# Performance work log

Measured on AMD Instinct MI355X. Metric: run time of the kernel, lower is better.

Reference implementation:

```python
import jax, jax.numpy as jnp
import numpy as np

N_NODES = 50000
N_EDGES = 800000
D_IN = 128
D_HID = 128


def _sage_conv(x, src, dst, W_l, b_l, W_r, num_nodes):
    # PyG SAGEConv (mean aggr): out = lin_l(mean_{j in N(i)} x_j) + lin_r(x_i)
    msgs = x[src]  # [E, d] irregular gather
    agg = jax.ops.segment_sum(msgs, dst, num_segments=num_nodes)  # [N, d]
    cnt = jax.ops.segment_sum(jnp.ones((dst.shape[0], 1), x.dtype), dst, num_segments=num_nodes)
    agg = agg / jnp.maximum(cnt, 1.0)  # mean over in-neighbors
    return agg @ W_l.T + b_l + x @ W_r.T


def setup_inputs() -> dict:
    key = jax.random.key(0)
    ks = jax.random.split(key, 8)
    x = jax.random.normal(ks[0], (N_NODES, D_IN), dtype=jnp.float32)
    edge_index = jax.random.randint(ks[1], (2, N_EDGES), 0, N_NODES, dtype=jnp.int64)
    s0 = 1.0 / np.sqrt(D_IN)
    s1 = 1.0 / np.sqrt(D_HID)
    return {
        "x": x,
        "edge_index": edge_index,
        "W_l0": jax.random.uniform(ks[2], (D_HID, D_IN), jnp.float32, -s0, s0),
        "b_l0": jnp.zeros((D_HID,), jnp.float32),
        "W_r0": jax.random.uniform(ks[3], (D_HID, D_IN), jnp.float32, -s0, s0),
        "W_l1": jax.random.uniform(ks[4], (D_HID, D_HID), jnp.float32, -s1, s1),
        "b_l1": jnp.zeros((D_HID,), jnp.float32),
        "W_r1": jax.random.uniform(ks[5], (D_HID, D_HID), jnp.float32, -s1, s1),
    }


def reference(x, edge_index, W_l0, b_l0, W_r0, W_l1, b_l1, W_r1):
    src, dst = edge_index[0], edge_index[1]
    n = x.shape[0]
    # layer 0 + ReLU (dropout is identity at inference)
    h = _sage_conv(x, src, dst, W_l0, b_l0, W_r0, n)
    h = jax.nn.relu(h)
    # layer 1 (no activation on last layer)
    out = _sage_conv(h, src, dst, W_l1, b_l1, W_r1, n)
    return out
```

## Files before the change

### kernel.cpp

```cpp
#include <hip/hip_runtime.h>


typedef __attribute__((ext_vector_type(8))) short short8;
typedef __attribute__((ext_vector_type(4))) float f32x4;

#define DEV __device__ __forceinline__

DEV unsigned short f2b(float f) {
  unsigned u = __builtin_bit_cast(unsigned, f);
  u += 0x7fffu + ((u >> 16) & 1u);
  return (unsigned short)(u >> 16);
}
DEV float b2f(unsigned short h) {
  unsigned u = ((unsigned)h) << 16;
  return __builtin_bit_cast(float, u);
}

constexpr int N_NODES = 50000;
constexpr int N_EDGES = 800000;
constexpr int D = 128;
constexpr int NBUCK = (N_NODES + 255) / 256;
constexpr int BCAP = 5120;
constexpr int EPB = (N_EDGES + NBUCK - 1) / NBUCK;
constexpr int NCONV = (N_NODES * D / 4) / 256;
constexpr int NPREP = (2 * 32 * 128) / 256;

__global__ __launch_bounds__(256) void setup_kernel(
    const float* __restrict__ x, unsigned short* __restrict__ xb,
    const float* __restrict__ Wl0, const float* __restrict__ Wr0,
    const float* __restrict__ Wl1, const float* __restrict__ Wr1,
    unsigned short* __restrict__ Bf,
    const int* __restrict__ src, const int* __restrict__ dst,
    int* __restrict__ g_bcnt, unsigned* __restrict__ staging) {
  __shared__ int cnt[NBUCK];
  __shared__ int cur[NBUCK];
  int bid = blockIdx.x;
  int t = threadIdx.x;

  if (bid < NCONV) {
    int i = bid * 256 + t;
    f32x4 v = ((const f32x4*)x)[i];
    uint2 o;
    o.x = (unsigned)f2b(v.x) | ((unsigned)f2b(v.y) << 16);
    o.y = (unsigned)f2b(v.z) | ((unsigned)f2b(v.w) << 16);
    ((uint2*)xb)[i] = o;
    return;
  }
  if (bid < NCONV + NPREP) {
    int f = (bid - NCONV) * 256 + t;
    int layer = f >> 12;
    int kchunk = (f >> 7) & 31;
    int n = f & 127;
    const float* W;
    if (layer == 0) W = (kchunk < 16) ? Wl0 : Wr0;
    else            W = (kchunk < 16) ? Wl1 : Wr1;
    int k = (kchunk & 15) * 8;
    const f32x4* row = (const f32x4*)(W + n * D + k);
    f32x4 a = row[0], b = row[1];
    uint4 pk;
    pk.x = (unsigned)f2b(a.x) | ((unsigned)f2b(a.y) << 16);
    pk.y = (unsigned)f2b(a.z) | ((unsigned)f2b(a.w) << 16);
    pk.z = (unsigned)f2b(b.x) | ((unsigned)f2b(b.y) << 16);
    pk.w = (unsigned)f2b(b.z) | ((unsigned)f2b(b.w) << 16);
    *(uint4*)(Bf + (size_t)f * 8) = pk;
    return;
  }

  int blk = bid - NCONV - NPREP;
  for (int i = t; i < NBUCK; i += 256) cnt[i] = 0;
  __syncthreads();
  int beg = blk * EPB;
  int end = min(beg + EPB, N_EDGES);
  for (int e = beg + t; e < end; e += 256) {
    atomicAdd(&cnt[dst[e] >> 8], 1);
  }
  __syncthreads();
  for (int i = t; i < NBUCK; i += 256) {
    cur[i] = atomicAdd(&g_bcnt[i], cnt[i]);
  }
  __syncthreads();
  for (int e = beg + t; e < end; e += 256) {
    int d = dst[e];
    int b = d >> 8;
    int p = atomicAdd(&cur[b], 1);
    if (p >= BCAP) p = BCAP - 1;
    staging[b * BCAP + p] = ((unsigned)(d & 255) << 16) | (unsigned)src[e];
  }
}

__global__ __launch_bounds__(256) void fill2_kernel(const unsigned* __restrict__ staging,
                                                    const int* __restrict__ g_bcnt,
                                                    int* __restrict__ offs,
                                                    int* __restrict__ csr) {
  __shared__ int cnts[256];
  __shared__ int tmp[256];
  __shared__ int hist[256];
  __shared__ int cur[256];
  int b = blockIdx.x;
  int t = threadIdx.x;
  int c = (t < NBUCK) ? g_bcnt[t] : 0;
  cnts[t] = c;
  tmp[t] = c;
  __syncthreads();
  for (int off = 1; off < 256; off <<= 1) {
    int u = (t >= off) ? tmp[t - off] : 0;
    __syncthreads();
    tmp[t] += u;
    __syncthreads();
  }
  int n = cnts[b];
  int bb = tmp[b] - n;
  if (b == 0 && t == 0) offs[N_NODES] = N_EDGES;

  const unsigned* st = staging + b * BCAP;
  hist[t] = 0;
  __syncthreads();
  for (int e = t; e < n; e += 256) atomicAdd(&hist[st[e] >> 16], 1);
  __syncthreads();
  int v = hist[t];
  tmp[t] = v;
  __syncthreads();
  for (int off = 1; off < 256; off <<= 1) {
    int u = (t >= off) ? tmp[t - off] : 0;
    __syncthreads();
    tmp[t] += u;
    __syncthreads();
  }
  int excl = tmp[t] - v;
  int node = b * 256 + t;
  if (node < N_NODES) offs[node] = bb + excl;
  cur[t] = bb + excl;
  __syncthreads();
  for (int e = t; e < n; e += 256) {
    unsigned pk = st[e];
    int p = atomicAdd(&cur[pk >> 16], 1);
    csr[p] = (int)(pk & 0xffffu);
  }
}

__global__ void agg_kernel(const unsigned short* __restrict__ feat,
                           const int* __restrict__ csr_src,
                           const int* __restrict__ offs,
                           unsigned short* __restrict__ out) {
  int w = (int)((blockIdx.x * blockDim.x + threadIdx.x) >> 6);
  int lane = threadIdx.x & 63;
  if (w >= N_NODES) return;
  int s = offs[w], e = offs[w + 1];
  const unsigned* f = (const unsigned*)feat;
  float ax = 0.f, ay = 0.f;
  int k = s;
  for (; k + 4 <= e; k += 4) {
    int s0 = csr_src[k], s1 = csr_src[k + 1], s2 = csr_src[k + 2], s3 = csr_src[k + 3];
    unsigned u0 = f[s0 * 64 + lane];
    unsigned u1 = f[s1 * 64 + lane];
    unsigned u2 = f[s2 * 64 + lane];
    unsigned u3 = f[s3 * 64 + lane];
    ax += b2f((unsigned short)u0) + b2f((unsigned short)u1) +
          b2f((unsigned short)u2) + b2f((unsigned short)u3);
    ay += b2f((unsigned short)(u0 >> 16)) + b2f((unsigned short)(u1 >> 16)) +
          b2f((unsigned short)(u2 >> 16)) + b2f((unsigned short)(u3 >> 16));
  }
  for (; k < e; ++k) {
    unsigned u = f[csr_src[k] * 64 + lane];
    ax += b2f((unsigned short)u);
    ay += b2f((unsigned short)(u >> 16));
  }
  float inv = 1.0f / (float)max(e - s, 1);
  unsigned o = (unsigned)f2b(ax * inv) | ((unsigned)f2b(ay * inv) << 16);
  ((unsigned*)out)[w * 64 + lane] = o;
}

__global__ __launch_bounds__(256) void gemm_kernel(
    const unsigned short* __restrict__ Aagg,
    const unsigned short* __restrict__ Afeat,
    const unsigned short* __restrict__ Bf,
    const float* __restrict__ bias,
    float* __restrict__ out_f32,
    unsigned short* __restrict__ out_bf16,
    int relu_bf16) {
  int wave = threadIdx.x >> 6;
  int lane = threadIdx.x & 63;
  int ml = lane & 15;
  int quad = lane >> 4;
  int node0 = blockIdx.x * 128 + wave * 32;

  int ar0 = node0 + ml;       if (ar0 >= N_NODES) ar0 = N_NODES - 1;
  int ar1 = node0 + 16 + ml;  if (ar1 >= N_NODES) ar1 = N_NODES - 1;

  f32x4 acc[2][8];
#pragma unroll
  for (int m = 0; m < 2; ++m)
#pragma unroll
    for (int t = 0; t < 8; ++t) acc[m][t] = (f32x4){0.f, 0.f, 0.f, 0.f};

  const short8* bf8 = (const short8*)Bf;
#pragma unroll
  for (int mat = 0; mat < 2; ++mat) {
    const unsigned short* A = mat ? Afeat : Aagg;
    const short8* a0 = (const short8*)(A + (size_t)ar0 * D);
    const short8* a1 = (const short8*)(A + (size_t)ar1 * D);
    int kbase = mat * 16;
#pragma unroll
    for (int kc = 0; kc < 4; ++kc) {
      short8 af0 = a0[kc * 4 + quad];
      short8 af1 = a1[kc * 4 + quad];
      const short8* brow = bf8 + (kbase + kc * 4 + quad) * 128;
#pragma unroll
      for (int nt = 0; nt < 8; ++nt) {
        short8 bfr = brow[nt * 16 + ml];
        acc[0][nt] = __builtin_amdgcn_mfma_f32_16x16x32_bf16(af0, bfr, acc[0][nt], 0, 0, 0);
        acc[1][nt] = __builtin_amdgcn_mfma_f32_16x16x32_bf16(af1, bfr, acc[1][nt], 0, 0, 0);
      }
    }
  }

#pragma unroll
  for (int tile = 0; tile < 2; ++tile) {
#pragma unroll
    for (int nt = 0; nt < 8; ++nt) {
      int col = nt * 16 + ml;
      float bv = bias[col];
#pragma unroll
      for (int r = 0; r < 4; ++r) {
        int node = node0 + tile * 16 + quad * 4 + r;
        if (node >= N_NODES) continue;
        float v = acc[tile][nt][r] + bv;
        if (relu_bf16) {
          v = v > 0.f ? v : 0.f;
          out_bf16[(size_t)node * D + col] = f2b(v);
        } else {
          out_f32[(size_t)node * D + col] = v;
        }
      }
    }
  }
}

extern "C" void kernel_launch(void* const* d_in, const int* in_sizes, int n_in,
                              void* d_out, int out_size, void* d_ws, size_t ws_size,
                              hipStream_t stream) {
  const float* x   = (const float*)d_in[0];
  const int*   ei  = (const int*)d_in[1];
  const float* Wl0 = (const float*)d_in[2];
  const float* bl0 = (const float*)d_in[3];
  const float* Wr0 = (const float*)d_in[4];
  const float* Wl1 = (const float*)d_in[5];
  const float* bl1 = (const float*)d_in[6];
  const float* Wr1 = (const float*)d_in[7];
  float* out = (float*)d_out;

  char* ws = (char*)d_ws;
  size_t o = 0;
  auto carve = [&](size_t bytes) {
    char* p = ws + o;
    o += bytes;
    o = (o + 255) & ~(size_t)255;
    return p;
  };
  int* offs       = (int*)carve((size_t)(N_NODES + 1) * 4);
  int* csr        = (int*)carve((size_t)N_EDGES * 4);
  int* g_bcnt     = (int*)carve((size_t)NBUCK * 4);
  unsigned* staging = (unsigned*)carve((size_t)NBUCK * BCAP * 4);
  unsigned short* Bf   = (unsigned short*)carve((size_t)2 * 32 * 128 * 8 * 2);
  unsigned short* xb   = (unsigned short*)carve((size_t)N_NODES * D * 2);
  unsigned short* aggb = (unsigned short*)carve((size_t)N_NODES * D * 2);
  unsigned short* hb   = (unsigned short*)carve((size_t)N_NODES * D * 2);

  const int* srcp = ei;
  const int* dstp = ei + N_EDGES;

  hipMemsetAsync(g_bcnt, 0, (size_t)NBUCK * 4, stream);
  setup_kernel<<<NCONV + NPREP + NBUCK, 256, 0, stream>>>(
      x, xb, Wl0, Wr0, Wl1, Wr1, Bf, srcp, dstp, g_bcnt, staging);
  fill2_kernel<<<NBUCK, 256, 0, stream>>>(staging, g_bcnt, offs, csr);

  const int GEMM_BLOCKS = (N_NODES + 127) / 128;
  agg_kernel<<<(N_NODES + 3) / 4, 256, 0, stream>>>(xb, csr, offs, aggb);
  gemm_kernel<<<GEMM_BLOCKS, 256, 0, stream>>>(aggb, xb, Bf, bl0, nullptr, hb, 1);
  agg_kernel<<<(N_NODES + 3) / 4, 256, 0, stream>>>(hb, csr, offs, aggb);
  gemm_kernel<<<GEMM_BLOCKS, 256, 0, stream>>>(aggb, hb, Bf + 32 * 128 * 8, bl1,
                                               out, nullptr, 0);
}
```

Measured before the change: 251.2 us.

## Spread edge binning over more blocks, schedule it first, widen CSR fill blocks

Edge binning moves from 196 blocks to 784 blocks and is placed at the start of the setup grid, so the atomic-heavy binning starts first and its per-block work drops. The fill kernel moves from 256 to 1024 threads per block, so 1024 threads run the histogram and scatter loops while only the first 256 do the scans. The other threads have to match every barrier in the scan code. More blocks also means more global atomics on the bucket counters.

```diff
diff --git a/kernel.cpp b/kernel.cpp
--- a/kernel.cpp
+++ b/kernel.cpp
@@ -21,7 +21,8 @@
 constexpr int D = 128;
 constexpr int NBUCK = (N_NODES + 255) / 256;
 constexpr int BCAP = 5120;
-constexpr int EPB = (N_EDGES + NBUCK - 1) / NBUCK;
+constexpr int NBIN = 784;
+constexpr int EPB = (N_EDGES + NBIN - 1) / NBIN;
 constexpr int NCONV = (N_NODES * D / 4) / 256;
 constexpr int NPREP = (2 * 32 * 128) / 256;
 
@@ -37,8 +38,30 @@
   int bid = blockIdx.x;
   int t = threadIdx.x;
 
-  if (bid < NCONV) {
-    int i = bid * 256 + t;
+  if (bid < NBIN) {
+    for (int i = t; i < NBUCK; i += 256) cnt[i] = 0;
+    __syncthreads();
+    int beg = bid * EPB;
+    int end = min(beg + EPB, N_EDGES);
+    for (int e = beg + t; e < end; e += 256) {
+      atomicAdd(&cnt[dst[e] >> 8], 1);
+    }
+    __syncthreads();
+    for (int i = t; i < NBUCK; i += 256) {
+      cur[i] = atomicAdd(&g_bcnt[i], cnt[i]);
+    }
+    __syncthreads();
+    for (int e = beg + t; e < end; e += 256) {
+      int d = dst[e];
+      int b = d >> 8;
+      int p = atomicAdd(&cur[b], 1);
+      if (p >= BCAP) p = BCAP - 1;
+      staging[b * BCAP + p] = ((unsigned)(d & 255) << 16) | (unsigned)src[e];
+    }
+    return;
+  }
+  if (bid < NBIN + NCONV) {
+    int i = (bid - NBIN) * 256 + t;
     f32x4 v = ((const f32x4*)x)[i];
     uint2 o;
     o.x = (unsigned)f2b(v.x) | ((unsigned)f2b(v.y) << 16);
@@ -46,92 +69,84 @@
     ((uint2*)xb)[i] = o;
     return;
   }
-  if (bid < NCONV + NPREP) {
-    int f = (bid - NCONV) * 256 + t;
-    int layer = f >> 12;
-    int kchunk = (f >> 7) & 31;
-    int n = f & 127;
-    const float* W;
-    if (layer == 0) W = (kchunk < 16) ? Wl0 : Wr0;
-    else            W = (kchunk < 16) ? Wl1 : Wr1;
-    int k = (kchunk & 15) * 8;
-    const f32x4* row = (const f32x4*)(W + n * D + k);
-    f32x4 a = row[0], b = row[1];
-    uint4 pk;
-    pk.x = (unsigned)f2b(a.x) | ((unsigned)f2b(a.y) << 16);
-    pk.y = (unsigned)f2b(a.z) | ((unsigned)f2b(a.w) << 16);
-    pk.z = (unsigned)f2b(b.x) | ((unsigned)f2b(b.y) << 16);
-    pk.w = (unsigned)f2b(b.z) | ((unsigned)f2b(b.w) << 16);
-    *(uint4*)(Bf + (size_t)f * 8) = pk;
-    return;
-  }
-
-  int blk = bid - NCONV - NPREP;
-  for (int i = t; i < NBUCK; i += 256) cnt[i] = 0;
-  __syncthreads();
-  int beg = blk * EPB;
-  int end = min(beg + EPB, N_EDGES);
-  for (int e = beg + t; e < end; e += 256) {
-    atomicAdd(&cnt[dst[e] >> 8], 1);
-  }
-  __syncthreads();
-  for (int i = t; i < NBUCK; i += 256) {
-    cur[i] = atomicAdd(&g_bcnt[i], cnt[i]);
-  }
-  __syncthreads();
-  for (int e = beg + t; e < end; e += 256) {
-    int d = dst[e];
-    int b = d >> 8;
-    int p = atomicAdd(&cur[b], 1);
-    if (p >= BCAP) p = BCAP - 1;
-    staging[b * BCAP + p] = ((unsigned)(d & 255) << 16) | (unsigned)src[e];
-  }
-}
-
-__global__ __launch_bounds__(256) void fill2_kernel(const unsigned* __restrict__ staging,
-                                                    const int* __restrict__ g_bcnt,
-                                                    int* __restrict__ offs,
-                                                    int* __restrict__ csr) {
+  int f = (bid - NBIN - NCONV) * 256 + t;
+  int layer = f >> 12;
+  int kchunk = (f >> 7) & 31;
+  int n = f & 127;
+  const float* W;
+  if (layer == 0) W = (kchunk < 16) ? Wl0 : Wr0;
+  else            W = (kchunk < 16) ? Wl1 : Wr1;
+  int k = (kchunk & 15) * 8;
+  const f32x4* row = (const f32x4*)(W + n * D + k);
+  f32x4 a = row[0], b = row[1];
+  uint4 pk;
+  pk.x = (unsigned)f2b(a.x) | ((unsigned)f2b(a.y) << 16);
+  pk.y = (unsigned)f2b(a.z) | ((unsigned)f2b(a.w) << 16);
+  pk.z = (unsigned)f2b(b.x) | ((unsigned)f2b(b.y) << 16);
+  pk.w = (unsigned)f2b(b.z) | ((unsigned)f2b(b.w) << 16);
+  *(uint4*)(Bf + (size_t)f * 8) = pk;
+}
+
+__global__ __launch_bounds__(1024) void fill2_kernel(const unsigned* __restrict__ staging,
+                                                     const int* __restrict__ g_bcnt,
+                                                     int* __restrict__ offs,
+                                                     int* __restrict__ csr) {
   __shared__ int cnts[256];
   __shared__ int tmp[256];
   __shared__ int hist[256];
   __shared__ int cur[256];
+  __shared__ int sh_n, sh_bb;
   int b = blockIdx.x;
   int t = threadIdx.x;
-  int c = (t < NBUCK) ? g_bcnt[t] : 0;
-  cnts[t] = c;
-  tmp[t] = c;
-  __syncthreads();
-  for (int off = 1; off < 256; off <<= 1) {
-    int u = (t >= off) ? tmp[t - off] : 0;
-    __syncthreads();
-    tmp[t] += u;
-    __syncthreads();
-  }
-  int n = cnts[b];
-  int bb = tmp[b] - n;
+  if (t < 256) {
+    int c = (t < NBUCK) ? g_bcnt[t] : 0;
+    cnts[t] = c;
+    tmp[t] = c;
+    hist[t] = 0;
+  }
+  __syncthreads();
+  if (t < 256) {
+    for (int off = 1; off < 256; off <<= 1) {
+      int u = (t >= off) ? tmp[t - off] : 0;
+      __syncthreads();
+      tmp[t] += u;
+      __syncthreads();
+    }
+  } else {
+    for (int off = 1; off < 256; off <<= 1) { __syncthreads(); __syncthreads(); }
+  }
+  if (t == 0) {
+    sh_n = cnts[b];
+    sh_bb = tmp[b] - cnts[b];
+  }
+  __syncthreads();
+  int n = sh_n;
+  int bb = sh_bb;
   if (b == 0 && t == 0) offs[N_NODES] = N_EDGES;
 
   const unsigned* st = staging + b * BCAP;
-  hist[t] = 0;
-  __syncthreads();
-  for (int e = t; e < n; e += 256) atomicAdd(&hist[st[e] >> 16], 1);
-  __syncthreads();
-  int v = hist[t];
-  tmp[t] = v;
-  __syncthreads();
-  for (int off = 1; off < 256; off <<= 1) {
-    int u = (t >= off) ? tmp[t - off] : 0;
-    __syncthreads();
-    tmp[t] += u;
-    __syncthreads();
-  }
-  int excl = tmp[t] - v;
-  int node = b * 256 + t;
-  if (node < N_NODES) offs[node] = bb + excl;
-  cur[t] = bb + excl;
-  __syncthreads();
-  for (int e = t; e < n; e += 256) {
+  for (int e = t; e < n; e += 1024) atomicAdd(&hist[st[e] >> 16], 1);
+  __syncthreads();
+  if (t < 256) {
+    int v = hist[t];
+    tmp[t] = v;
+    __syncthreads();
+    for (int off = 1; off < 256; off <<= 1) {
+      int u = (t >= off) ? tmp[t - off] : 0;
+      __syncthreads();
+      tmp[t] += u;
+      __syncthreads();
+    }
+    int excl = tmp[t] - v;
+    int node = b * 256 + t;
+    if (node < N_NODES) offs[node] = bb + excl;
+    cur[t] = bb + excl;
+  } else {
+    __syncthreads();
+    for (int off = 1; off < 256; off <<= 1) { __syncthreads(); __syncthreads(); }
+  }
+  __syncthreads();
+  for (int e = t; e < n; e += 1024) {
     unsigned pk = st[e];
     int p = atomicAdd(&cur[pk >> 16], 1);
     csr[p] = (int)(pk & 0xffffu);
@@ -270,9 +285,9 @@
   const int* dstp = ei + N_EDGES;
 
   hipMemsetAsync(g_bcnt, 0, (size_t)NBUCK * 4, stream);
-  setup_kernel<<<NCONV + NPREP + NBUCK, 256, 0, stream>>>(
+  setup_kernel<<<NBIN + NCONV + NPREP, 256, 0, stream>>>(
       x, xb, Wl0, Wr0, Wl1, Wr1, Bf, srcp, dstp, g_bcnt, staging);
-  fill2_kernel<<<NBUCK, 256, 0, stream>>>(staging, g_bcnt, offs, csr);
+  fill2_kernel<<<NBUCK, 1024, 0, stream>>>(staging, g_bcnt, offs, csr);
 
   const int GEMM_BLOCKS = (N_NODES + 127) / 128;
   agg_kernel<<<(N_NODES + 3) / 4, 256, 0, stream>>>(xb, csr, offs, aggb);
```

After: 240.9 us. 1.04x faster.
